# Optimization experiments

Measured on AMD Instinct MI355X. Metric: run time of the kernel, lower is better.

Reference implementation:

```python
import jax, jax.numpy as jnp
import numpy as np

# --- static config matching init_kwargs ---
L = 6            # discretization level -> 2^L Euler substeps per unit time
T = 10           # number of time units
N = 1000         # number of particles
DX = 16          # state dim (== obs dim)
INIT_VAL = 0.0
SUB = 2 ** L
HL = 2.0 ** (-L)
S = SUB * T + 1  # total path length


def setup_inputs() -> dict:
    key = jax.random.key(0)
    k1, k2, k3, k4 = jax.random.split(key, 4)
    input_path = jax.random.normal(k1, (S, DX), dtype=jnp.float32) * 0.1
    observe_path = jax.random.normal(k2, (T + 1, DX), dtype=jnp.float32) * 0.5
    # stable linear drift mu(x) = x @ A.T, constant diffusion matrix Sig
    A = (-0.5 * jnp.eye(DX) + 0.05 * jax.random.normal(k3, (DX, DX))).astype(jnp.float32)
    Sig = (0.3 * jnp.eye(DX) + 0.02 * jax.random.normal(k4, (DX, DX))).astype(jnp.float32)
    return {"input_path": input_path, "observe_path": observe_path, "A": A, "Sig": Sig}


def _mu(x, A):
    return x @ A.T


def _llg(x, y):
    # Gaussian observation log-likelihood per particle: x (N,DX), y (DX,)
    return -0.5 * jnp.sum((y - x) ** 2, axis=-1)


def _euler_segment(x0, A, Sig, key):
    # unit_path_update: 2^L Euler-Maruyama steps; returns (SUB, N, DX)
    dw = jax.random.normal(key, (SUB, x0.shape[0], DX)) * np.sqrt(HL).astype(np.float32)
    def step(x, d):
        xn = x + _mu(x, A) * HL + d @ Sig.T
        return xn, xn
    _, seg = jax.lax.scan(step, x0, dw)
    return seg


def _multinomial_idx(wn, dice):
    bins = jnp.cumsum(wn)
    bins = bins.at[-1].set(jnp.maximum(1.0, bins[-1]))  # bins[-1] = max(1, bins[-1])
    return jnp.clip(jnp.searchsorted(bins, dice, side="right"), 0, N - 1)


def _forward(input_path, observe_path, A, Sig):
    key = jax.random.key(42)
    un = jnp.full((S, N, DX), INIT_VAL, dtype=input_path.dtype)
    un_hat = jnp.full((S, N, DX), INIT_VAL, dtype=input_path.dtype)
    gn = jnp.zeros((N,), dtype=input_path.dtype)
    wn = jnp.full((N,), 1.0 / N, dtype=input_path.dtype)
    for t in range(T):  # static unroll over time units (indices are static)
        start, upd = SUB * t, SUB * (t + 1)
        kdw = jax.random.fold_in(key, 2 * t)
        kres = jax.random.fold_in(key, 2 * t + 1)
        un = un.at[: start + 1].set(un_hat[: start + 1])
        seg = _euler_segment(un[start], A, Sig, kdw)
        un = un.at[start + 1 : upd + 1].set(seg)
        un = un.at[:, -1, :].set(input_path)  # pin conditioned path as last particle
        gn = _llg(un[upd], observe_path[t + 1]) + gn
        wn = jax.nn.softmax(gn)  # exp(gn - max)/sum, numerically stable
        ess = 1.0 / jnp.sum(wn ** 2)
        do_rs = ess <= N / 2
        idx = _multinomial_idx(wn, jax.random.uniform(kres, (N,)))
        prefix = un[: upd + 1]
        gathered = prefix[:, idx, :]
        new_prefix = jnp.where(do_rs, gathered, prefix)
        gn = jnp.where(do_rs, jnp.zeros_like(gn), gn)
        un_hat = un_hat.at[: upd + 1].set(new_prefix)
        un_hat = un_hat.at[:, -1, :].set(input_path)
    # sample_output: draw one particle index from final weights
    kfin = jax.random.fold_in(key, 2 * T)
    i0 = _multinomial_idx(wn, jax.random.uniform(kfin, (1,)))[0]
    return un[:, i0, :]  # (S, DX)


def reference(input_path, observe_path, A, Sig):
    return _forward(input_path, observe_path, A, Sig)
```

## Files before the change

### kernel.cpp

```cpp
#include <hip/hip_runtime.h>
#include <cstdint>
#include <cstddef>

#pragma clang fp contract(off)


typedef unsigned int u32;

#define NP   1000
#define DXC  16
#define SUBC 64
#define TC   10
#define SC   641

#define WS_XS   0
#define WS_ANC  160000
#define WS_XF0  170032
#define WS_XF1  186032
#define WS_GN0  202032
#define WS_GN1  203032
#define WS_DSG  204032

__device__ __forceinline__ u32 rotl32(u32 v, u32 d) { return (v << d) | (v >> (32u - d)); }

__device__ __forceinline__ void tf2x32(u32 k0, u32 k1, u32 c0, u32 c1, u32& o0, u32& o1) {
  u32 ks0 = k0, ks1 = k1, ks2 = k0 ^ k1 ^ 0x1BD11BDAu;
  u32 x0 = c0 + ks0, x1 = c1 + ks1;
  x0 += x1; x1 = rotl32(x1,13); x1 ^= x0;
  x0 += x1; x1 = rotl32(x1,15); x1 ^= x0;
  x0 += x1; x1 = rotl32(x1,26); x1 ^= x0;
  x0 += x1; x1 = rotl32(x1, 6); x1 ^= x0;
  x0 += ks1; x1 += ks2 + 1u;
  x0 += x1; x1 = rotl32(x1,17); x1 ^= x0;
  x0 += x1; x1 = rotl32(x1,29); x1 ^= x0;
  x0 += x1; x1 = rotl32(x1,16); x1 ^= x0;
  x0 += x1; x1 = rotl32(x1,24); x1 ^= x0;
  x0 += ks2; x1 += ks0 + 2u;
  x0 += x1; x1 = rotl32(x1,13); x1 ^= x0;
  x0 += x1; x1 = rotl32(x1,15); x1 ^= x0;
  x0 += x1; x1 = rotl32(x1,26); x1 ^= x0;
  x0 += x1; x1 = rotl32(x1, 6); x1 ^= x0;
  x0 += ks0; x1 += ks1 + 3u;
  x0 += x1; x1 = rotl32(x1,17); x1 ^= x0;
  x0 += x1; x1 = rotl32(x1,29); x1 ^= x0;
  x0 += x1; x1 = rotl32(x1,16); x1 ^= x0;
  x0 += x1; x1 = rotl32(x1,24); x1 ^= x0;
  x0 += ks1; x1 += ks2 + 4u;
  x0 += x1; x1 = rotl32(x1,13); x1 ^= x0;
  x0 += x1; x1 = rotl32(x1,15); x1 ^= x0;
  x0 += x1; x1 = rotl32(x1,26); x1 ^= x0;
  x0 += x1; x1 = rotl32(x1, 6); x1 ^= x0;
  x0 += ks2; x1 += ks0 + 5u;
  o0 = x0; o1 = x1;
}

__device__ __forceinline__ u32 bits32p(u32 k0, u32 k1, u32 i) {
  u32 o0, o1; tf2x32(k0, k1, 0u, i, o0, o1); return o0 ^ o1;
}

__device__ __forceinline__ float u01(u32 b) {
  return __uint_as_float((b >> 9) | 0x3f800000u) - 1.0f;
}

__device__ __forceinline__ float xla_exp(float input) {
#pragma clang fp contract(off)
  float x = fminf(input, 88.3762626647950f);
  x = fmaxf(x, -88.3762626647949f);
  float fx = floorf(__builtin_fmaf(x, 1.44269504088896341f, 0.5f));
  float tmp = 0.693359375f * fx;
  float z0  = -2.12194440e-4f * fx;
  float xr = x - tmp;
  xr = xr - z0;
  float z = xr * xr;
  float y = __builtin_fmaf(xr, 1.9875691500e-4f, 1.3981999507e-3f);
  y = __builtin_fmaf(y, xr, 8.3334519073e-3f);
  y = __builtin_fmaf(y, xr, 4.1665795894e-2f);
  y = __builtin_fmaf(y, xr, 1.6666665459e-1f);
  y = __builtin_fmaf(y, xr, 5.0000001201e-1f);
  y = __builtin_fmaf(y, z, xr);
  y = 1.0f + y;
  int n = (int)fx;
  float p2n = __uint_as_float((u32)(n + 127) << 23);
  float res = y * p2n;
  return fmaxf(res, input);
}

__device__ __forceinline__ float xla_log(float input) {
#pragma clang fp contract(off)
  float t0 = fmaxf(input, __uint_as_float(0x00800000u));
  u32 bi = __float_as_uint(t0);
  float e = (float)(int)((bi >> 23) - 126u);
  float x = __uint_as_float((bi & 0x807fffffu) | 0x3f000000u);
  float mo, mx;
  if (x < 0.707106781186547524f) { mx = x; mo = 1.0f; } else { mx = 0.0f; mo = 0.0f; }
  x = x - 1.0f;
  e = e - mo;
  x = x + mx;
  float z = x * x;
  float y = __builtin_fmaf(x, 7.0376836292e-2f, -1.1514610310e-1f);
  y = __builtin_fmaf(y, x, 1.1676998740e-1f);
  y = __builtin_fmaf(y, x, -1.2420140846e-1f);
  y = __builtin_fmaf(y, x, 1.4249322787e-1f);
  y = __builtin_fmaf(y, x, -1.6668057665e-1f);
  y = __builtin_fmaf(y, x, 2.0000714765e-1f);
  y = __builtin_fmaf(y, x, -2.4999993993e-1f);
  y = __builtin_fmaf(y, x, 3.3333331174e-1f);
  y = y * x;
  y = y * z;
  y = __builtin_fmaf(e, -2.12194440e-4f, y);
  y = y - 0.5f * z;
  x = x + y;
  x = __builtin_fmaf(e, 0.693359375f, x);
  return x;
}

__device__ __forceinline__ float xla_log1p(float x) {
#pragma clang fp contract(off)
  float ax = fabsf(x);
  if (ax < 1e-4f) {
    float t = (-0.5f * x) + 1.0f;
    return t * x;
  }
  return xla_log(x + 1.0f);
}

__device__ __forceinline__ float xla_erfinv(float u) {
#pragma clang fp contract(off)
  float w = -xla_log1p((-u) * u);
  float p;
  if (w < 5.0f) {
    float ww = w - 2.5f;
    p = 2.81022636e-08f;
    p = 3.43273939e-07f  + p * ww;
    p = -3.5233877e-06f  + p * ww;
    p = -4.39150654e-06f + p * ww;
    p = 0.00021858087f   + p * ww;
    p = -0.00125372503f  + p * ww;
    p = -0.00417768164f  + p * ww;
    p = 0.246640727f     + p * ww;
    p = 1.50140941f      + p * ww;
  } else {
    float ww = (float)__builtin_sqrt((double)w) - 3.0f;
    p = -0.000200214257f;
    p = 0.000100950558f + p * ww;
    p = 0.00134934322f  + p * ww;
    p = -0.00367342844f + p * ww;
    p = 0.00573950773f  + p * ww;
    p = -0.0076224613f  + p * ww;
    p = 0.00943887047f  + p * ww;
    p = 1.00167406f     + p * ww;
    p = 2.83297682f     + p * ww;
  }
  return p * u;
}

#define U_LO __uint_as_float(0xBF7FFFFFu)

__device__ __forceinline__ float nrm(u32 bits) {
#pragma clang fp contract(off)
  float f = u01(bits);
  float u = (f * 2.0f) + U_LO;
  u = fmaxf(U_LO, u);
  return __uint_as_float(0x3FB504F3u) * xla_erfinv(u);
}

__device__ __forceinline__ void gen_unit(int t, int blk, int tid,
                                         const float* __restrict__ Sg_s,
                                         float* __restrict__ wsf) {
#pragma clang fp contract(off)
  int nl = tid & 7;
  int s  = tid >> 3;
  int n  = blk * 8 + nl;
  int gtid = (t * 125 + blk) * 512 + tid;
  u32 k0, k1; tf2x32(0u, 42u, 0u, (u32)(2 * t), k0, k1);
  float dwv[DXC];
#pragma unroll
  for (int k = 0; k < DXC; ++k) {
    u32 b = bits32p(k0, k1, (u32)(s * 16000 + n * 16 + k));
    dwv[k] = nrm(b) * 0.125f;
  }
  float* dst = wsf + WS_DSG + (size_t)gtid * 16;
#pragma unroll
  for (int d = 0; d < DXC; ++d) {
    float dg = 0.0f;
#pragma unroll
    for (int k = 0; k < DXC; ++k) dg = __builtin_fmaf(dwv[k], Sg_s[d * 16 + k], dg);
    dst[d] = dg;
  }
}

__device__ void cumsum_tree_par(const float* x0, float* out0, float* scr, int tid) {
#pragma clang fp contract(off)
  const int nlv[10] = {1000, 500, 250, 125, 62, 31, 15, 7, 3, 1};
  const float* raw[10]; float* scn[10]; float* rawm[10];
  raw[0] = x0; scn[0] = out0;
  int off = 0;
  for (int k = 1; k < 10; ++k) {
    rawm[k] = scr + off; raw[k] = rawm[k]; off += nlv[k];
    scn[k] = scr + off; off += nlv[k];
  }
  for (int k = 0; k < 9; ++k) {
    int nr = nlv[k + 1];
    for (int i = tid; i < nr; i += 512) rawm[k + 1][i] = raw[k][2 * i] + raw[k][2 * i + 1];
    __syncthreads();
  }
  if (tid == 0) scn[9][0] = raw[9][0];
  __syncthreads();
  for (int k = 8; k >= 0; --k) {
    int nk = nlv[k], nr = nlv[k + 1];
    if (tid == 0) scn[k][0] = raw[k][0];
    for (int i = tid; i < nr; i += 512) scn[k][2 * i + 1] = scn[k + 1][i];
    if ((nk & 1) == 0) {
      for (int i = 1 + tid; i < nr; i += 512) scn[k][2 * i] = scn[k + 1][i - 1] + raw[k][2 * i];
    } else {
      for (int i = 1 + tid; i <= nr; i += 512) scn[k][2 * i] = scn[k + 1][i - 1] + raw[k][2 * i];
    }
    __syncthreads();
  }
}

__device__ void filter_step(int s, const float* __restrict__ inp,
                            const float* __restrict__ obs,
                            float* __restrict__ wsf, int tid, int wr,
                            float* gn_s, float* e_s, float* wn_s, float* bins_s,
                            float* scr_s, float* red_s, int* src_s, float* sh) {
#pragma clang fp contract(off)
  const float* XFp = wsf + ((s & 1) ? WS_XF1 : WS_XF0);
  const float* GNp = wsf + (((s & 1) ^ 1) ? WS_GN1 : WS_GN0);
  float* GNw = wsf + ((s & 1) ? WS_GN1 : WS_GN0);
  int* ANC = (int*)(wsf + WS_ANC);
  int upd = SUBC * (s + 1);

  for (int n = tid; n < NP; n += 512) {
    float sacc = 0.0f;
    for (int d = 0; d < DXC; ++d) {
      float fv = (n == NP - 1) ? inp[upd * 16 + d] : XFp[n * 16 + d];
      float dd = obs[(s + 1) * 16 + d] - fv;
      float sq = dd * dd;
      sacc = sacc + sq;
    }
    float gp = (s == 0) ? 0.0f : GNp[n];
    gn_s[n] = (-0.5f * sacc) + gp;
  }
  __syncthreads();
  {
    float mv = -__builtin_inff();
    for (int n = tid; n < NP; n += 512) mv = fmaxf(mv, gn_s[n]);
#pragma unroll
    for (int off = 32; off >= 1; off >>= 1) mv = fmaxf(mv, __shfl_xor(mv, off));
    if ((tid & 63) == 0) red_s[tid >> 6] = mv;
    __syncthreads();
    if (tid == 0) {
      float a = fmaxf(fmaxf(red_s[0], red_s[1]), fmaxf(red_s[2], red_s[3]));
      float b = fmaxf(fmaxf(red_s[4], red_s[5]), fmaxf(red_s[6], red_s[7]));
      sh[0] = fmaxf(a, b);
    }
    __syncthreads();
  }
  float m = sh[0];
  for (int n = tid; n < NP; n += 512) e_s[n] = xla_exp(gn_s[n] - m);
  __syncthreads();
  if (tid < 8) {
    float a = 0.0f;
    for (int i = 0; i < 125; ++i) a = a + e_s[i * 8 + tid];
    red_s[tid] = a;
  }
  __syncthreads();
  if (tid == 0) {
    float b0 = red_s[0] + red_s[4], b1 = red_s[1] + red_s[5],
          b2 = red_s[2] + red_s[6], b3 = red_s[3] + red_s[7];
    float c0 = b0 + b2, c1 = b1 + b3;
    sh[1] = c0 + c1;
  }
  __syncthreads();
  float ssum = sh[1];
  for (int n = tid; n < NP; n += 512) wn_s[n] = e_s[n] / ssum;
  __syncthreads();
  if (tid < 8) {
    float a = 0.0f;
    for (int i = 0; i < 125; ++i) { float v = wn_s[i * 8 + tid]; float q = v * v; a = a + q; }
    red_s[tid] = a;
  }
  __syncthreads();
  if (tid == 0) {
    float b0 = red_s[0] + red_s[4], b1 = red_s[1] + red_s[5],
          b2 = red_s[2] + red_s[6], b3 = red_s[3] + red_s[7];
    float c0 = b0 + b2, c1 = b1 + b3;
    float ss = c0 + c1;
    float ess = 1.0f / ss;
    sh[2] = (ess <= 500.0f) ? 1.0f : 0.0f;
  }
  __syncthreads();
  cumsum_tree_par(wn_s, bins_s, scr_s, tid);
  if (tid == 0) bins_s[NP - 1] = fmaxf(1.0f, bins_s[NP - 1]);
  __syncthreads();
  int rs = (sh[2] != 0.0f);
  u32 kr0, kr1; tf2x32(0u, 42u, 0u, (u32)(2 * s + 1), kr0, kr1);
  for (int n = tid; n < NP; n += 512) {
    u32 b = bits32p(kr0, kr1, (u32)n);
    float dice = fmaxf(0.0f, u01(b));
    int lo = 0, hi = NP;
    while (lo < hi) { int mid = (lo + hi) >> 1; if (bins_s[mid] <= dice) lo = mid + 1; else hi = mid; }
    int idx = lo > NP - 1 ? NP - 1 : lo;
    int a = rs ? idx : n;
    src_s[n] = (n == NP - 1) ? (NP - 1) : a;
    if (wr) {
      ANC[s * NP + n] = a;
      GNw[n] = rs ? 0.0f : gn_s[n];
    }
  }
  __syncthreads();
}

__global__ __launch_bounds__(512, 1) void k_gen0(const float* __restrict__ Sg,
                                                 float* __restrict__ wsf) {
  __shared__ float Sg_s[256];
  int tid = threadIdx.x;
  if (tid < 256) Sg_s[tid] = Sg[tid];
  __syncthreads();
  gen_unit(0, (int)blockIdx.x, tid, Sg_s, wsf);
}

__global__ __launch_bounds__(512, 1) void k_step(const float* __restrict__ inp,
                                                 const float* __restrict__ obs,
                                                 const float* __restrict__ A,
                                                 const float* __restrict__ Sg,
                                                 float* __restrict__ wsf, int t) {
#pragma clang fp contract(off)
  __shared__ float dsg_s[8192];
  __shared__ float gn_s[NP], e_s[NP], wn_s[NP], bins_s[NP], scr_s[2048];
  __shared__ float red_s[8], sh[4];
  __shared__ int src_s[NP];
  int tid = threadIdx.x;
  int bid = (int)blockIdx.x;
  if (bid >= 125) {
    if (t >= TC - 1) return;
    __shared__ float Sg_s[256];
    if (tid < 256) Sg_s[tid] = Sg[tid];
    __syncthreads();
    gen_unit(t + 1, bid - 125, tid, Sg_s, wsf);
    return;
  }
  int base = bid * 8;
  const float* DSG = wsf + WS_DSG + (size_t)t * 1024000 + (size_t)bid * 8192;
#pragma unroll
  for (int j = 0; j < 16; ++j) dsg_s[j * 512 + tid] = DSG[j * 512 + tid];
  if (t > 0) {
    filter_step(t - 1, inp, obs, wsf, tid, bid == 0,
                gn_s, e_s, wn_s, bins_s, scr_s, red_s, src_s, sh);
  } else {
    __syncthreads();
  }
  if (tid < 128) {
    int p = tid >> 4, d = tid & 15;
    int n = base + p;
    float Ar[DXC];
#pragma unroll
    for (int k = 0; k < DXC; ++k) Ar[k] = A[d * 16 + k];
    float x = 0.0f;
    if (t > 0) {
      const float* XFp = wsf + (((t - 1) & 1) ? WS_XF1 : WS_XF0);
      int s0 = src_s[n];
      x = (s0 == NP - 1) ? inp[(SUBC * t) * 16 + d] : XFp[s0 * 16 + d];
    }
    wsf[WS_XS + t * 16000 + n * 16 + d] = x;
    for (int sl = 0; sl < SUBC; ++sl) {
      float mu = 0.0f;
#pragma unroll
      for (int k = 0; k < DXC; ++k) {
        float xk = __shfl(x, k, 16);
        mu = __builtin_fmaf(xk, Ar[k], mu);
      }
      float t2 = x + mu * 0.015625f;
      x = t2 + dsg_s[sl * 128 + p * 16 + d];
    }
    float* XFc = wsf + ((t & 1) ? WS_XF1 : WS_XF0);
    XFc[n * 16 + d] = x;
  }
}

__global__ __launch_bounds__(512, 1) void k_out(const float* __restrict__ inp,
                                                const float* __restrict__ obs,
                                                const float* __restrict__ A,
                                                float* __restrict__ wsf,
                                                float* __restrict__ out) {
#pragma clang fp contract(off)
  __shared__ float gn_s[NP], e_s[NP], wn_s[NP], bins_s[NP], scr_s[2048];
  __shared__ float red_s[8], sh[4];
  __shared__ int src_s[NP];
  __shared__ float dsg_t[1024];
  __shared__ int lin_s[24];
  int tid = threadIdx.x;
  int bid = (int)blockIdx.x;
  filter_step(TC - 1, inp, obs, wsf, tid, 0,
              gn_s, e_s, wn_s, bins_s, scr_s, red_s, src_s, sh);
  if (tid == 0) {
    const int* ANC = (const int*)(wsf + WS_ANC);
    u32 kf0, kf1; tf2x32(0u, 42u, 0u, (u32)(2 * TC), kf0, kf1);
    u32 b = bits32p(kf0, kf1, 0u);
    float dice = fmaxf(0.0f, u01(b));
    int lo = 0, hi = NP;
    while (lo < hi) { int mid = (lo + hi) >> 1; if (bins_s[mid] <= dice) lo = mid + 1; else hi = mid; }
    int i0 = lo > NP - 1 ? NP - 1 : lo;
    lin_s[0] = i0;
    lin_s[1 + 9] = i0;
    int hit = (i0 == NP - 1) ? 1 : 0;
    lin_s[11 + 9] = hit;
    int j = i0;
    for (int u = 8; u >= 0; --u) {
      j = ANC[u * NP + j];
      if (j == NP - 1) hit = 1;
      lin_s[1 + u] = j;
      lin_s[11 + u] = hit;
    }
  }
  __syncthreads();
  int i0 = lin_s[0];
  int i = bid * 512 + tid;
  if (i < SC * DXC) {
    int srow = i >> 4;
    if (i0 == NP - 1) out[i] = inp[i];
    else if (srow == 0) out[i] = lin_s[11 + 0] ? inp[i] : 0.0f;
    else { int u = (srow - 1) >> 6; if (lin_s[11 + u]) out[i] = inp[i]; }
  }
  if (bid >= TC) return;
  if (i0 == NP - 1) return;
  int u = bid;
  if (lin_s[11 + u]) return;
  int p = lin_s[1 + u];
  const float* DSG = wsf + WS_DSG + (size_t)u * 1024000 + (size_t)(p >> 3) * 8192
                     + (size_t)(p & 7) * 16;
  {
    int idx = tid;
    int sl = idx >> 4, d = idx & 15;
    dsg_t[idx] = DSG[sl * 128 + d];
    idx = 512 + tid;
    sl = idx >> 4; d = idx & 15;
    dsg_t[idx] = DSG[sl * 128 + d];
  }
  __syncthreads();
  if (tid < 16) {
    int d = tid;
    float Ar[DXC];
#pragma unroll
    for (int k = 0; k < DXC; ++k) Ar[k] = A[d * 16 + k];
    float x = wsf[WS_XS + u * 16000 + p * 16 + d];
    for (int sl = 0; sl < SUBC; ++sl) {
      float mu = 0.0f;
#pragma unroll
      for (int k = 0; k < DXC; ++k) {
        float xk = __shfl(x, k, 16);
        mu = __builtin_fmaf(xk, Ar[k], mu);
      }
      float t2 = x + mu * 0.015625f;
      x = t2 + dsg_t[sl * 16 + d];
      out[(u * SUBC + sl + 1) * DXC + d] = x;
    }
  }
}

extern "C" void kernel_launch(void* const* d_in, const int* in_sizes, int n_in,
                              void* d_out, int out_size, void* d_ws, size_t ws_size,
                              hipStream_t stream) {
  (void)in_sizes; (void)n_in; (void)out_size; (void)ws_size;
  const float* inp = (const float*)d_in[0];
  const float* obs = (const float*)d_in[1];
  const float* A   = (const float*)d_in[2];
  const float* Sg  = (const float*)d_in[3];
  float* wsf = (float*)d_ws;
  float* out = (float*)d_out;

  k_gen0<<<dim3(125), dim3(512), 0, stream>>>(Sg, wsf);
  for (int t = 0; t < TC; ++t) {
    k_step<<<dim3(250), dim3(512), 0, stream>>>(inp, obs, A, Sg, wsf, t);
  }
  k_out<<<dim3(21), dim3(512), 0, stream>>>(inp, obs, A, wsf, out);
}
```

Measured before the change: 311.3 us.

## Fuse per-timestep kernel launches into one cooperative persistent kernel with grid sync

Replaces the 12 separate kernel launches (generation, ten step kernels, output) with a single cooperative kernel of 250 blocks that loops over time units and separates them with grid-wide syncs. Noise generation for unit t+2 runs on the spare blocks while the other blocks do step t, and both unit 0 and unit 1 are generated up front. The intent is to remove launch overhead and inter-kernel gaps. In exchange, 250 blocks must be co-resident, and the fused kernel's larger shared-memory footprint plus grid-sync cost may offset the gain.

Result: slower. 1.059 ms (+240.3%).

```diff
diff --git a/kernel.cpp b/kernel.cpp
--- a/kernel.cpp
+++ b/kernel.cpp
@@ -1,8 +1,11 @@
 #include <hip/hip_runtime.h>
+#include <hip/hip_cooperative_groups.h>
 #include <cstdint>
 #include <cstddef>
 
 #pragma clang fp contract(off)
+
+namespace cg = cooperative_groups;
 
 
 typedef unsigned int u32;
@@ -312,79 +315,16 @@
   __syncthreads();
 }
 
-__global__ __launch_bounds__(512, 1) void k_gen0(const float* __restrict__ Sg,
-                                                 float* __restrict__ wsf) {
-  __shared__ float Sg_s[256];
-  int tid = threadIdx.x;
-  if (tid < 256) Sg_s[tid] = Sg[tid];
-  __syncthreads();
-  gen_unit(0, (int)blockIdx.x, tid, Sg_s, wsf);
-}
-
-__global__ __launch_bounds__(512, 1) void k_step(const float* __restrict__ inp,
-                                                 const float* __restrict__ obs,
-                                                 const float* __restrict__ A,
-                                                 const float* __restrict__ Sg,
-                                                 float* __restrict__ wsf, int t) {
-#pragma clang fp contract(off)
-  __shared__ float dsg_s[8192];
-  __shared__ float gn_s[NP], e_s[NP], wn_s[NP], bins_s[NP], scr_s[2048];
-  __shared__ float red_s[8], sh[4];
-  __shared__ int src_s[NP];
-  int tid = threadIdx.x;
-  int bid = (int)blockIdx.x;
-  if (bid >= 125) {
-    if (t >= TC - 1) return;
-    __shared__ float Sg_s[256];
-    if (tid < 256) Sg_s[tid] = Sg[tid];
-    __syncthreads();
-    gen_unit(t + 1, bid - 125, tid, Sg_s, wsf);
-    return;
-  }
-  int base = bid * 8;
-  const float* DSG = wsf + WS_DSG + (size_t)t * 1024000 + (size_t)bid * 8192;
-#pragma unroll
-  for (int j = 0; j < 16; ++j) dsg_s[j * 512 + tid] = DSG[j * 512 + tid];
-  if (t > 0) {
-    filter_step(t - 1, inp, obs, wsf, tid, bid == 0,
-                gn_s, e_s, wn_s, bins_s, scr_s, red_s, src_s, sh);
-  } else {
-    __syncthreads();
-  }
-  if (tid < 128) {
-    int p = tid >> 4, d = tid & 15;
-    int n = base + p;
-    float Ar[DXC];
-#pragma unroll
-    for (int k = 0; k < DXC; ++k) Ar[k] = A[d * 16 + k];
-    float x = 0.0f;
-    if (t > 0) {
-      const float* XFp = wsf + (((t - 1) & 1) ? WS_XF1 : WS_XF0);
-      int s0 = src_s[n];
-      x = (s0 == NP - 1) ? inp[(SUBC * t) * 16 + d] : XFp[s0 * 16 + d];
-    }
-    wsf[WS_XS + t * 16000 + n * 16 + d] = x;
-    for (int sl = 0; sl < SUBC; ++sl) {
-      float mu = 0.0f;
-#pragma unroll
-      for (int k = 0; k < DXC; ++k) {
-        float xk = __shfl(x, k, 16);
-        mu = __builtin_fmaf(xk, Ar[k], mu);
-      }
-      float t2 = x + mu * 0.015625f;
-      x = t2 + dsg_s[sl * 128 + p * 16 + d];
-    }
-    float* XFc = wsf + ((t & 1) ? WS_XF1 : WS_XF0);
-    XFc[n * 16 + d] = x;
-  }
-}
-
-__global__ __launch_bounds__(512, 1) void k_out(const float* __restrict__ inp,
+__global__ __launch_bounds__(512, 1) void k_all(const float* __restrict__ inp,
                                                 const float* __restrict__ obs,
                                                 const float* __restrict__ A,
+                                                const float* __restrict__ Sg,
                                                 float* __restrict__ wsf,
                                                 float* __restrict__ out) {
 #pragma clang fp contract(off)
+  cg::grid_group grid = cg::this_grid();
+  __shared__ float Sg_s[256];
+  __shared__ float dsg_s[8192];
   __shared__ float gn_s[NP], e_s[NP], wn_s[NP], bins_s[NP], scr_s[2048];
   __shared__ float red_s[8], sh[4];
   __shared__ int src_s[NP];
@@ -392,6 +332,57 @@
   __shared__ int lin_s[24];
   int tid = threadIdx.x;
   int bid = (int)blockIdx.x;
+  if (tid < 256) Sg_s[tid] = Sg[tid];
+  __syncthreads();
+  if (bid < 125) gen_unit(0, bid, tid, Sg_s, wsf);
+  else gen_unit(1, bid - 125, tid, Sg_s, wsf);
+  __threadfence();
+  grid.sync();
+  for (int t = 0; t < TC; ++t) {
+    if (bid >= 125) {
+      if (t + 2 < TC) gen_unit(t + 2, bid - 125, tid, Sg_s, wsf);
+    } else {
+      int base = bid * 8;
+      const float* DSG = wsf + WS_DSG + (size_t)t * 1024000 + (size_t)bid * 8192;
+#pragma unroll
+      for (int j = 0; j < 16; ++j) dsg_s[j * 512 + tid] = DSG[j * 512 + tid];
+      if (t > 0) {
+        filter_step(t - 1, inp, obs, wsf, tid, bid == 0,
+                    gn_s, e_s, wn_s, bins_s, scr_s, red_s, src_s, sh);
+      } else {
+        __syncthreads();
+      }
+      if (tid < 128) {
+        int p = tid >> 4, d = tid & 15;
+        int n = base + p;
+        float Ar[DXC];
+#pragma unroll
+        for (int k = 0; k < DXC; ++k) Ar[k] = A[d * 16 + k];
+        float x = 0.0f;
+        if (t > 0) {
+          const float* XFp = wsf + (((t - 1) & 1) ? WS_XF1 : WS_XF0);
+          int s0 = src_s[n];
+          x = (s0 == NP - 1) ? inp[(SUBC * t) * 16 + d] : XFp[s0 * 16 + d];
+        }
+        wsf[WS_XS + t * 16000 + n * 16 + d] = x;
+        for (int sl = 0; sl < SUBC; ++sl) {
+          float mu = 0.0f;
+#pragma unroll
+          for (int k = 0; k < DXC; ++k) {
+            float xk = __shfl(x, k, 16);
+            mu = __builtin_fmaf(xk, Ar[k], mu);
+          }
+          float t2 = x + mu * 0.015625f;
+          x = t2 + dsg_s[sl * 128 + p * 16 + d];
+        }
+        float* XFc = wsf + ((t & 1) ? WS_XF1 : WS_XF0);
+        XFc[n * 16 + d] = x;
+      }
+    }
+    __threadfence();
+    grid.sync();
+  }
+  if (bid >= 21) return;
   filter_step(TC - 1, inp, obs, wsf, tid, 0,
               gn_s, e_s, wn_s, bins_s, scr_s, red_s, src_s, sh);
   if (tid == 0) {
@@ -470,9 +461,8 @@
   float* wsf = (float*)d_ws;
   float* out = (float*)d_out;
 
-  k_gen0<<<dim3(125), dim3(512), 0, stream>>>(Sg, wsf);
-  for (int t = 0; t < TC; ++t) {
-    k_step<<<dim3(250), dim3(512), 0, stream>>>(inp, obs, A, Sg, wsf, t);
-  }
-  k_out<<<dim3(21), dim3(512), 0, stream>>>(inp, obs, A, wsf, out);
-}
+  void* args[] = { (void*)&inp, (void*)&obs, (void*)&A, (void*)&Sg,
+                   (void*)&wsf, (void*)&out };
+  hipLaunchCooperativeKernel((const void*)k_all, dim3(250), dim3(512),
+                             args, 0, stream);
+}
```

## Fuse noise gen into first step, precompute log-likelihoods, overlap DSG load with filter

Applied to the files above, without the earlier changes.

Drops the separate k_gen0 launch: at t=0 the step blocks generate their own noise increments in registers and write them to both shared memory and the workspace. Each step kernel now computes the per-particle Gaussian observation log-likelihood right after the Euler loop, using a shuffle reduction, and stores it in workspace. The next filter step reads that value instead of recomputing it redundantly from the final states in every block. The DSG load is issued into registers before the filter step so its latency can hide behind the filter work, at the cost of extra register pressure.

Measured after the change: 311.7 us. About the same (+0.1%).

```diff
diff --git a/kernel.cpp b/kernel.cpp
--- a/kernel.cpp
+++ b/kernel.cpp
@@ -19,7 +19,9 @@
 #define WS_XF1  186032
 #define WS_GN0  202032
 #define WS_GN1  203032
-#define WS_DSG  204032
+#define WS_LG0  204032
+#define WS_LG1  205032
+#define WS_DSG  206032
 
 __device__ __forceinline__ u32 rotl32(u32 v, u32 d) { return (v << d) | (v >> (32u - d)); }
 
@@ -164,29 +166,38 @@
   return __uint_as_float(0x3FB504F3u) * xla_erfinv(u);
 }
 
+__device__ __forceinline__ void gen_vals(int t, int blk, int tid,
+                                         const float* __restrict__ Sg_s,
+                                         float* __restrict__ dg) {
+#pragma clang fp contract(off)
+  int nl = tid & 7;
+  int s  = tid >> 3;
+  int n  = blk * 8 + nl;
+  u32 k0, k1; tf2x32(0u, 42u, 0u, (u32)(2 * t), k0, k1);
+  float dwv[DXC];
+#pragma unroll
+  for (int k = 0; k < DXC; ++k) {
+    u32 b = bits32p(k0, k1, (u32)(s * 16000 + n * 16 + k));
+    dwv[k] = nrm(b) * 0.125f;
+  }
+#pragma unroll
+  for (int d = 0; d < DXC; ++d) {
+    float g = 0.0f;
+#pragma unroll
+    for (int k = 0; k < DXC; ++k) g = __builtin_fmaf(dwv[k], Sg_s[d * 16 + k], g);
+    dg[d] = g;
+  }
+}
+
 __device__ __forceinline__ void gen_unit(int t, int blk, int tid,
                                          const float* __restrict__ Sg_s,
                                          float* __restrict__ wsf) {
-#pragma clang fp contract(off)
-  int nl = tid & 7;
-  int s  = tid >> 3;
-  int n  = blk * 8 + nl;
+  float dg[DXC];
+  gen_vals(t, blk, tid, Sg_s, dg);
   int gtid = (t * 125 + blk) * 512 + tid;
-  u32 k0, k1; tf2x32(0u, 42u, 0u, (u32)(2 * t), k0, k1);
-  float dwv[DXC];
-#pragma unroll
-  for (int k = 0; k < DXC; ++k) {
-    u32 b = bits32p(k0, k1, (u32)(s * 16000 + n * 16 + k));
-    dwv[k] = nrm(b) * 0.125f;
-  }
   float* dst = wsf + WS_DSG + (size_t)gtid * 16;
 #pragma unroll
-  for (int d = 0; d < DXC; ++d) {
-    float dg = 0.0f;
-#pragma unroll
-    for (int k = 0; k < DXC; ++k) dg = __builtin_fmaf(dwv[k], Sg_s[d * 16 + k], dg);
-    dst[d] = dg;
-  }
+  for (int d = 0; d < DXC; ++d) dst[d] = dg[d];
 }
 
 __device__ void cumsum_tree_par(const float* x0, float* out0, float* scr, int tid) {
@@ -219,28 +230,21 @@
   }
 }
 
-__device__ void filter_step(int s, const float* __restrict__ inp,
-                            const float* __restrict__ obs,
+__device__ void filter_step(int s, const float* __restrict__ obs,
                             float* __restrict__ wsf, int tid, int wr,
                             float* gn_s, float* e_s, float* wn_s, float* bins_s,
                             float* scr_s, float* red_s, int* src_s, float* sh) {
 #pragma clang fp contract(off)
-  const float* XFp = wsf + ((s & 1) ? WS_XF1 : WS_XF0);
+  const float* LLGp = wsf + ((s & 1) ? WS_LG1 : WS_LG0);
   const float* GNp = wsf + (((s & 1) ^ 1) ? WS_GN1 : WS_GN0);
   float* GNw = wsf + ((s & 1) ? WS_GN1 : WS_GN0);
   int* ANC = (int*)(wsf + WS_ANC);
-  int upd = SUBC * (s + 1);
+  (void)obs;
 
   for (int n = tid; n < NP; n += 512) {
-    float sacc = 0.0f;
-    for (int d = 0; d < DXC; ++d) {
-      float fv = (n == NP - 1) ? inp[upd * 16 + d] : XFp[n * 16 + d];
-      float dd = obs[(s + 1) * 16 + d] - fv;
-      float sq = dd * dd;
-      sacc = sacc + sq;
-    }
+    float l = LLGp[n];
     float gp = (s == 0) ? 0.0f : GNp[n];
-    gn_s[n] = (-0.5f * sacc) + gp;
+    gn_s[n] = l + gp;
   }
   __syncthreads();
   {
@@ -312,21 +316,13 @@
   __syncthreads();
 }
 
-__global__ __launch_bounds__(512, 1) void k_gen0(const float* __restrict__ Sg,
-                                                 float* __restrict__ wsf) {
-  __shared__ float Sg_s[256];
-  int tid = threadIdx.x;
-  if (tid < 256) Sg_s[tid] = Sg[tid];
-  __syncthreads();
-  gen_unit(0, (int)blockIdx.x, tid, Sg_s, wsf);
-}
-
 __global__ __launch_bounds__(512, 1) void k_step(const float* __restrict__ inp,
                                                  const float* __restrict__ obs,
                                                  const float* __restrict__ A,
                                                  const float* __restrict__ Sg,
                                                  float* __restrict__ wsf, int t) {
 #pragma clang fp contract(off)
+  __shared__ float Sg_s[256];
   __shared__ float dsg_s[8192];
   __shared__ float gn_s[NP], e_s[NP], wn_s[NP], bins_s[NP], scr_s[2048];
   __shared__ float red_s[8], sh[4];
@@ -334,21 +330,35 @@
   int tid = threadIdx.x;
   int bid = (int)blockIdx.x;
   if (bid >= 125) {
-    if (t >= TC - 1) return;
-    __shared__ float Sg_s[256];
+    if (t + 1 < TC) {
+      if (tid < 256) Sg_s[tid] = Sg[tid];
+      __syncthreads();
+      gen_unit(t + 1, bid - 125, tid, Sg_s, wsf);
+    }
+    return;
+  }
+  int base = bid * 8;
+  if (t == 0) {
     if (tid < 256) Sg_s[tid] = Sg[tid];
     __syncthreads();
-    gen_unit(t + 1, bid - 125, tid, Sg_s, wsf);
-    return;
-  }
-  int base = bid * 8;
-  const float* DSG = wsf + WS_DSG + (size_t)t * 1024000 + (size_t)bid * 8192;
-#pragma unroll
-  for (int j = 0; j < 16; ++j) dsg_s[j * 512 + tid] = DSG[j * 512 + tid];
-  if (t > 0) {
-    filter_step(t - 1, inp, obs, wsf, tid, bid == 0,
+    float dg[DXC];
+    gen_vals(0, bid, tid, Sg_s, dg);
+    float* dst = wsf + WS_DSG + ((size_t)bid * 512 + tid) * 16;
+#pragma unroll
+    for (int d = 0; d < DXC; ++d) {
+      dst[d] = dg[d];
+      dsg_s[tid * 16 + d] = dg[d];
+    }
+    __syncthreads();
+  } else {
+    float r[16];
+    const float* DSG = wsf + WS_DSG + (size_t)t * 1024000 + (size_t)bid * 8192;
+#pragma unroll
+    for (int j = 0; j < 16; ++j) r[j] = DSG[j * 512 + tid];
+    filter_step(t - 1, obs, wsf, tid, bid == 0,
                 gn_s, e_s, wn_s, bins_s, scr_s, red_s, src_s, sh);
-  } else {
+#pragma unroll
+    for (int j = 0; j < 16; ++j) dsg_s[j * 512 + tid] = r[j];
     __syncthreads();
   }
   if (tid < 128) {
@@ -376,6 +386,20 @@
     }
     float* XFc = wsf + ((t & 1) ? WS_XF1 : WS_XF0);
     XFc[n * 16 + d] = x;
+    int upd = SUBC * (t + 1);
+    float fv = (n == NP - 1) ? inp[upd * 16 + d] : x;
+    float dd = obs[(t + 1) * 16 + d] - fv;
+    float sacc = 0.0f;
+#pragma unroll
+    for (int k = 0; k < DXC; ++k) {
+      float v = __shfl(dd, k, 16);
+      float sq = v * v;
+      sacc = sacc + sq;
+    }
+    if (d == 0) {
+      float* LLGw = wsf + ((t & 1) ? WS_LG1 : WS_LG0);
+      LLGw[n] = -0.5f * sacc;
+    }
   }
 }
 
@@ -392,7 +416,7 @@
   __shared__ int lin_s[24];
   int tid = threadIdx.x;
   int bid = (int)blockIdx.x;
-  filter_step(TC - 1, inp, obs, wsf, tid, 0,
+  filter_step(TC - 1, obs, wsf, tid, 0,
               gn_s, e_s, wn_s, bins_s, scr_s, red_s, src_s, sh);
   if (tid == 0) {
     const int* ANC = (const int*)(wsf + WS_ANC);
@@ -470,7 +494,6 @@
   float* wsf = (float*)d_ws;
   float* out = (float*)d_out;
 
-  k_gen0<<<dim3(125), dim3(512), 0, stream>>>(Sg, wsf);
   for (int t = 0; t < TC; ++t) {
     k_step<<<dim3(250), dim3(512), 0, stream>>>(inp, obs, A, Sg, wsf, t);
   }
```
